# Optimization experiments

Measured on AMD Instinct MI355X. Metric: run time of the kernel, lower is better.

## Reference

```python
import jax, jax.numpy as jnp
import numpy as np
import math

# ---- config (mirrors FastRCNNRoIHeads init args) ----
B, N, C = 8, 2048, 2            # images, proposals/img, classes (incl. background)
K = 100                          # detections_per_img
IMG_H, IMG_W = 512, 512
SCORE_THRESH = 0.05
NMS_THRESH = 0.4
MIN_SIZE = 0.01
WX, WY, WW, WH = 10.0, 10.0, 5.0, 5.0   # BoxCoder weights
BBOX_XFORM_CLIP = math.log(1000.0 / 16.0)


def setup_inputs() -> dict:
    key = jax.random.key(0)
    k1, k2, k3, k4, k5 = jax.random.split(key, 5)
    prop_clss = jax.random.normal(k1, (B, N, C), dtype=jnp.float32)
    prop_regs = 0.1 * jax.random.normal(k2, (B, N, 4), dtype=jnp.float32)
    prop_qlts = jax.random.normal(k3, (B, N, 1), dtype=jnp.float32)
    # valid proposal boxes inside the image: x1,y1 in [0,448), w,h in [16,128)
    xy1 = jax.random.uniform(k4, (B, N, 2), dtype=jnp.float32) * 380.0
    wh = 16.0 + jax.random.uniform(k5, (B, N, 2), dtype=jnp.float32) * 112.0
    props = jnp.concatenate([xy1, xy1 + wh], axis=-1)
    return {"prop_clss": prop_clss, "prop_regs": prop_regs,
            "prop_qlts": prop_qlts, "props": props}


def _decode(regs, props):
    # torchvision BoxCoder.decode_single, class-agnostic [N,4] deltas
    w = props[:, 2] - props[:, 0]
    h = props[:, 3] - props[:, 1]
    cx = props[:, 0] + 0.5 * w
    cy = props[:, 1] + 0.5 * h
    dx, dy = regs[:, 0] / WX, regs[:, 1] / WY
    dw = jnp.minimum(regs[:, 2] / WW, BBOX_XFORM_CLIP)
    dh = jnp.minimum(regs[:, 3] / WH, BBOX_XFORM_CLIP)
    pcx, pcy = dx * w + cx, dy * h + cy
    pw, ph = jnp.exp(dw) * w, jnp.exp(dh) * h
    return jnp.stack([pcx - 0.5 * pw, pcy - 0.5 * ph,
                      pcx + 0.5 * pw, pcy + 0.5 * ph], axis=-1)


def _iou_matrix(b):
    area = (b[:, 2] - b[:, 0]) * (b[:, 3] - b[:, 1])
    lt = jnp.maximum(b[:, None, :2], b[None, :, :2])
    rb = jnp.minimum(b[:, None, 2:], b[None, :, 2:])
    wh = jnp.clip(rb - lt, 0.0)
    inter = wh[..., 0] * wh[..., 1]
    return inter / (area[:, None] + area[None, :] - inter + 1e-9)


def _postprocess_one(clss, regs, qlts, props):
    boxes = _decode(regs, props)
    boxes = jnp.stack([jnp.clip(boxes[:, 0], 0.0, IMG_W),
                       jnp.clip(boxes[:, 1], 0.0, IMG_H),
                       jnp.clip(boxes[:, 2], 0.0, IMG_W),
                       jnp.clip(boxes[:, 3], 0.0, IMG_H)], axis=-1)
    small_ok = ((boxes[:, 2] - boxes[:, 0]) >= MIN_SIZE) & \
               ((boxes[:, 3] - boxes[:, 1]) >= MIN_SIZE)
    raw = jax.nn.softmax(clss, axis=-1)[:, 1:]          # [N, C-1]
    q = jax.nn.sigmoid(qlts[:, 0])                      # [N]
    scores = (q[:, None] * raw).reshape(-1)             # [N*(C-1)]
    raw_f = raw.reshape(-1)
    Cm1 = C - 1
    M = N * Cm1
    prop_idx = jnp.arange(M) // Cm1
    cls_idx = jnp.arange(M) % Cm1 + 1
    valid = (raw_f > SCORE_THRESH) & small_ok[prop_idx]
    cand_boxes = boxes[prop_idx]                        # [M,4]
    # batched_nms: offset boxes per class so NMS runs per class
    max_coord = jnp.max(cand_boxes)
    boxes_off = cand_boxes + (cls_idx.astype(boxes.dtype) * (max_coord + 1.0))[:, None]
    masked = jnp.where(valid, scores, -1.0)
    order = jnp.argsort(-masked)
    b_s = cand_boxes[order]
    bo_s = boxes_off[order]
    s_s = scores[order]
    c_s = cls_idx[order]
    v_s = valid[order]
    iou = _iou_matrix(bo_s)                             # [M,M]
    idxs = jnp.arange(M)

    def step(keep, i):
        sup = (iou[i] > NMS_THRESH) & (idxs > i)
        keep = jnp.where(keep[i], keep & ~sup, keep)
        return keep, None

    keep, _ = jax.lax.scan(step, v_s, idxs)
    rank = jnp.cumsum(keep.astype(jnp.int32)) - 1
    dest = jnp.where(keep & (rank < K), rank, K)        # K = dump slot
    out_b = jnp.zeros((K + 1, 4), boxes.dtype).at[dest].set(b_s)[:K]
    out_s = jnp.zeros((K + 1,), boxes.dtype).at[dest].set(s_s)[:K]
    out_c = jnp.zeros((K + 1,), jnp.int32).at[dest].set(c_s.astype(jnp.int32))[:K]
    return out_b, out_s, out_c


def reference(prop_clss, prop_regs, prop_qlts, props):
    boxes, scores, classes = jax.vmap(_postprocess_one)(
        prop_clss, prop_regs, prop_qlts, props)
    return boxes, scores, classes
```

## Files before the change

### kernel.cpp

```cpp
#include <hip/hip_runtime.h>
#include <stdint.h>

#define NPROP 2048
#define NCLS  2
#define KDET  100
#define BT    512
#define NMS_TH 0.4f

__device__ __forceinline__ float dec_score(uint64_t k) {
    uint32_t u = ~(uint32_t)(k >> 32);
    uint32_t bits = (u & 0x80000000u) ? (u & 0x7FFFFFFFu) : ~u;
    return __uint_as_float(bits);
}

__device__ __forceinline__ float bcastf(float v, int srclane) {
    return __uint_as_float((uint32_t)__builtin_amdgcn_readlane(__float_as_int(v), srclane));
}

__device__ __forceinline__ void decode_one(
    const float* __restrict__ clss, const float* __restrict__ regs,
    const float* __restrict__ qlts, const float* __restrict__ props,
    int b, int i, float4& boxOut, uint64_t& keyOut, float& mxOut)
{
    const float CLIPV = 4.135166556742356f;
    float4 p  = ((const float4*)props)[b * NPROP + i];
    float4 rg = ((const float4*)regs)[b * NPROP + i];
    float2 cc = ((const float2*)clss)[b * NPROP + i];
    float  qv = qlts[(size_t)b * NPROP + i];

    float w  = __fsub_rn(p.z, p.x);
    float h  = __fsub_rn(p.w, p.y);
    float cx = __fadd_rn(p.x, __fmul_rn(0.5f, w));
    float cy = __fadd_rn(p.y, __fmul_rn(0.5f, h));
    float dx = __fdiv_rn(rg.x, 10.0f);
    float dy = __fdiv_rn(rg.y, 10.0f);
    float dw = fminf(__fdiv_rn(rg.z, 5.0f), CLIPV);
    float dh = fminf(__fdiv_rn(rg.w, 5.0f), CLIPV);
    float pcx = __fadd_rn(__fmul_rn(dx, w), cx);
    float pcy = __fadd_rn(__fmul_rn(dy, h), cy);
    float pw  = __fmul_rn(expf(dw), w);
    float ph  = __fmul_rn(expf(dh), h);
    float x1 = __fsub_rn(pcx, __fmul_rn(0.5f, pw));
    float y1 = __fsub_rn(pcy, __fmul_rn(0.5f, ph));
    float x2 = __fadd_rn(pcx, __fmul_rn(0.5f, pw));
    float y2 = __fadd_rn(pcy, __fmul_rn(0.5f, ph));
    x1 = fminf(fmaxf(x1, 0.0f), 512.0f);
    y1 = fminf(fmaxf(y1, 0.0f), 512.0f);
    x2 = fminf(fmaxf(x2, 0.0f), 512.0f);
    y2 = fminf(fmaxf(y2, 0.0f), 512.0f);
    bool small_ok = (__fsub_rn(x2, x1) >= 0.01f) && (__fsub_rn(y2, y1) >= 0.01f);

    float m  = fmaxf(cc.x, cc.y);
    float e0 = expf(__fsub_rn(cc.x, m));
    float e1 = expf(__fsub_rn(cc.y, m));
    float raw = __fdiv_rn(e1, __fadd_rn(e0, e1));
    float sq  = __fdiv_rn(1.0f, __fadd_rn(1.0f, expf(-qv)));
    float score = __fmul_rn(sq, raw);
    bool valid = (raw > 0.05f) && small_ok;
    float masked = valid ? score : -1.0f;

    boxOut = make_float4(x1, y1, x2, y2);
    uint32_t fb = __float_as_uint(masked);
    uint32_t u  = (fb & 0x80000000u) ? ~fb : (fb | 0x80000000u);
    keyOut = ((uint64_t)(~u) << 32) | (uint32_t)i;
    mxOut = fmaxf(fmaxf(x1, y1), fmaxf(x2, y2));
}

__device__ __forceinline__ void bitonic2048(uint64_t key[4], uint64_t* skey,
                                            int idxBase, int lane)
{
    for (int k = 2; k <= NPROP; k <<= 1) {
        for (int j = k >> 1; j > 0; j >>= 1) {
            if (j >= 256) {
                __syncthreads();
#pragma unroll
                for (int r = 0; r < 4; ++r) {
                    int idx = idxBase + r;
                    skey[(idx >> 2) | ((idx & 3) << 9)] = key[r];
                }
                __syncthreads();
#pragma unroll
                for (int r = 0; r < 4; ++r) {
                    int idx  = idxBase + r;
                    int pidx = idx ^ j;
                    uint64_t o = skey[(pidx >> 2) | ((pidx & 3) << 9)];
                    bool takeMin = (((idx & k) == 0) == ((idx & j) == 0));
                    bool lt = key[r] < o;
                    uint64_t mn = lt ? key[r] : o, mx = lt ? o : key[r];
                    key[r] = takeMin ? mn : mx;
                }
            } else if (j >= 4) {
                int lx = j >> 2;
#pragma unroll
                for (int r = 0; r < 4; ++r) {
                    int idx = idxBase + r;
                    uint64_t o = __shfl_xor(key[r], lx, 64);
                    bool takeMin = (((idx & k) == 0) == ((lane & lx) == 0));
                    bool lt = key[r] < o;
                    uint64_t mn = lt ? key[r] : o, mx = lt ? o : key[r];
                    key[r] = takeMin ? mn : mx;
                }
            } else {
#pragma unroll
                for (int r = 0; r < 4; ++r) {
                    if ((r & j) == 0) {
                        int rh = r | j;
                        int idx = idxBase + r;
                        bool up = ((idx & k) == 0);
                        uint64_t a = key[r], c2 = key[rh];
                        bool lt = a < c2;
                        uint64_t mn = lt ? a : c2, mx = lt ? c2 : a;
                        key[r] = up ? mn : mx; key[rh] = up ? mx : mn;
                    }
                }
            }
        }
    }
}

__device__ __forceinline__ int phaseC(
    const uint64_t* keys, int nv, const float4* sboxp, float off,
    uint64_t* s_colpart, uint64_t* s_inpart, float4* s_kbox, float* s_karea,
    int* s_keep, int* s_kept, int lane, int wv)
{
    int c = 0;
    while (true) {
        __syncthreads();
        int kept = *s_kept;
        if (c >= nv || kept >= KDET) break;
        int W = min(64, nv - c);
        bool have = (lane < W);

        float qx1 = 0.f, qy1 = 0.f, qx2 = 0.f, qy2 = 0.f, qa = 0.f;
        if (have) {
            float4 bx = sboxp[(uint32_t)keys[c + lane]];
            qx1 = __fadd_rn(bx.x, off); qy1 = __fadd_rn(bx.y, off);
            qx2 = __fadd_rn(bx.z, off); qy2 = __fadd_rn(bx.w, off);
            qa  = __fmul_rn(__fsub_rn(qx2, qx1), __fsub_rn(qy2, qy1));
        }

        uint64_t colpart = 0;
#pragma unroll
        for (int t = 0; t < 8; ++t) {
            int i = wv + (t << 3);
            bool rowok = (i < W);
            int isrc = rowok ? i : 0;
            float rx1 = bcastf(qx1, isrc);
            float ry1 = bcastf(qy1, isrc);
            float rx2 = bcastf(qx2, isrc);
            float ry2 = bcastf(qy2, isrc);
            float ra  = bcastf(qa , isrc);
            float ltx = fmaxf(rx1, qx1), lty = fmaxf(ry1, qy1);
            float rbx = fminf(rx2, qx2), rby = fminf(ry2, qy2);
            float iw = fmaxf(__fsub_rn(rbx, ltx), 0.0f);
            float ih = fmaxf(__fsub_rn(rby, lty), 0.0f);
            float inter = __fmul_rn(iw, ih);
            float denom = __fadd_rn(__fsub_rn(__fadd_rn(ra, qa), inter), 1e-9f);
            float iou   = __fdiv_rn(inter, denom);
            bool pred = rowok && have && (lane > i) && (iou > NMS_TH);
            uint64_t bm = (uint64_t)__ballot(pred);
            colpart |= ((bm >> lane) & 1ull) << isrc;
        }
        s_colpart[(wv << 6) | lane] = colpart;

        bool supin = false;
        if (have && kept) {
            for (int ki = wv; ki < kept; ki += 8) {
                float4 ko = s_kbox[ki];
                float  ka = s_karea[ki];
                float ltx = fmaxf(ko.x, qx1), lty = fmaxf(ko.y, qy1);
                float rbx = fminf(ko.z, qx2), rby = fminf(ko.w, qy2);
                float iw = fmaxf(__fsub_rn(rbx, ltx), 0.0f);
                float ih = fmaxf(__fsub_rn(rby, lty), 0.0f);
                float inter = __fmul_rn(iw, ih);
                float denom = __fadd_rn(__fsub_rn(__fadd_rn(ka, qa), inter), 1e-9f);
                supin = supin || (__fdiv_rn(inter, denom) > NMS_TH);
            }
        }
        uint64_t inb = (uint64_t)__ballot(supin);
        if (lane == 0) s_inpart[wv] = inb;
        __syncthreads();

        if (wv == 0) {
            uint64_t col = 0, insup = 0;
#pragma unroll
            for (int w2 = 0; w2 < 8; ++w2) {
                col   |= s_colpart[(w2 << 6) | lane];
                insup |= s_inpart[w2];
            }
            bool aliveBit = have && !((insup >> lane) & 1ull);
            uint64_t keepM = (uint64_t)__ballot(aliveBit);
            for (int it = 0; it < 64; ++it) {
                uint64_t nk = (uint64_t)__ballot(aliveBit && ((col & keepM) == 0ull));
                if (nk == keepM) break;
                keepM = nk;
            }
            int quota = KDET - kept;
            int nNew  = __popcll(keepM);
            int take  = nNew < quota ? nNew : quota;
            uint64_t below = keepM & ~(~0ull << lane);
            int rank = __popcll(below);
            bool mine = (((keepM >> lane) & 1ull) != 0ull) && (rank < quota);
            if (mine) {
                s_keep[kept + rank]  = c + lane;
                s_kbox[kept + rank]  = make_float4(qx1, qy1, qx2, qy2);
                s_karea[kept + rank] = qa;
            }
            if (lane == 0) *s_kept = kept + take;
        }
        c += 64;
    }
    __syncthreads();
    return *s_kept;
}

__global__ __launch_bounds__(BT) void PRISM_71511205479155_kernel(
    const float* __restrict__ clss, const float* __restrict__ regs,
    const float* __restrict__ qlts, const float* __restrict__ props,
    float* __restrict__ out, int B)
{
    __shared__ float4   sbox[NPROP];
    __shared__ uint64_t skey[NPROP];
    __shared__ uint64_t cand[512];
    __shared__ uint32_t hist[1024];
    __shared__ uint64_t s_colpart[8 * 64];
    __shared__ uint64_t s_inpart[8];
    __shared__ float4   s_kbox[KDET];
    __shared__ float    s_karea[KDET];
    __shared__ int      s_keep[KDET];
    __shared__ int      s_wsum[8];
    __shared__ int      s_maxc, s_kept, s_beta, s_M, s_totV, s_cnt, s_fb;

    const int b = blockIdx.x, tid = threadIdx.x, lane = tid & 63, wv = tid >> 6;
    const int idxBase = (wv << 8) | (lane << 2);

    hist[tid] = 0; hist[tid + 512] = 0;
    cand[tid] = ~0ull;
    if (tid == 0) { s_maxc = 0; s_kept = 0; s_beta = -1; s_M = 0; s_totV = 0; s_cnt = 0; s_fb = 0; }
    __syncthreads();

    uint64_t key[4];
    float thmax = 0.0f;
#pragma unroll
    for (int r = 0; r < 4; ++r) {
        int i = idxBase + r;
        float4 bx; uint64_t k; float mx;
        decode_one(clss, regs, qlts, props, b, i, bx, k, mx);
        sbox[i] = bx; skey[i] = k; key[r] = k;
        thmax = fmaxf(thmax, mx);
        uint32_t bkt = (uint32_t)(k >> 53);
        if (bkt < 1024)
            atomicAdd(&hist[bkt >> 1], (bkt & 1) ? 0x10000u : 1u);
    }
#pragma unroll
    for (int d = 1; d < 64; d <<= 1) thmax = fmaxf(thmax, __shfl_xor(thmax, d, 64));
    if (lane == 0) atomicMax(&s_maxc, __float_as_int(thmax));
    __syncthreads();

    {
        uint32_t w0 = hist[2 * tid], w1 = hist[2 * tid + 1];
        uint32_t c0 = w0 & 0xFFFFu, c1 = w0 >> 16, c2 = w1 & 0xFFFFu, c3 = w1 >> 16;
        uint32_t local = c0 + c1 + c2 + c3;
        uint32_t incl = local;
#pragma unroll
        for (int d = 1; d < 64; d <<= 1) {
            uint32_t v = __shfl_up(incl, d, 64);
            if (lane >= d) incl += v;
        }
        if (lane == 63) s_wsum[wv] = (int)incl;
        __syncthreads();
        int base = 0, tot = 0;
#pragma unroll
        for (int w = 0; w < 8; ++w) {
            int sv = s_wsum[w];
            tot += sv;
            if (w < wv) base += sv;
        }
        int target = tot < 256 ? tot : 256;
        uint32_t run = (uint32_t)base + incl - local;
        uint32_t cc[4] = {c0, c1, c2, c3};
#pragma unroll
        for (int r = 0; r < 4; ++r) {
            uint32_t ci = run + cc[r];
            if (target > 0 && (int)run < target && (int)ci >= target) {
                s_beta = 4 * tid + r;
                s_M = (int)ci;
                if (ci > 512) s_fb = 1;
            }
            run = ci;
        }
        if (tid == 0) s_totV = tot;
        __syncthreads();
    }

    const float off = __fadd_rn(__int_as_float(s_maxc), 1.0f);
    const int beta = s_beta, M = s_M, totV = s_totV;
    int fb = s_fb;

    if (!fb) {
#pragma unroll
        for (int r = 0; r < 4; ++r) {
            if ((int)(key[r] >> 53) <= beta) {
                int p = atomicAdd(&s_cnt, 1);
                cand[p] = key[r];
            }
        }
        __syncthreads();

        if (wv == 0) {
            uint64_t q[8];
#pragma unroll
            for (int r = 0; r < 8; ++r) q[r] = cand[(lane << 3) | r];
            for (int k2 = 2; k2 <= 512; k2 <<= 1) {
                for (int j = k2 >> 1; j > 0; j >>= 1) {
                    if (j >= 8) {
                        int lx = j >> 3;
#pragma unroll
                        for (int r = 0; r < 8; ++r) {
                            int idx = (lane << 3) | r;
                            uint64_t o = __shfl_xor(q[r], lx, 64);
                            bool takeMin = (((idx & k2) == 0) == ((idx & j) == 0));
                            bool lt = q[r] < o;
                            uint64_t mn = lt ? q[r] : o, mx = lt ? o : q[r];
                            q[r] = takeMin ? mn : mx;
                        }
                    } else {
#pragma unroll
                        for (int r = 0; r < 8; ++r) {
                            if ((r & j) == 0) {
                                int rh = r | j;
                                int idx = (lane << 3) | r;
                                bool up = ((idx & k2) == 0);
                                uint64_t a = q[r], c2 = q[rh];
                                bool lt = a < c2;
                                uint64_t mn = lt ? a : c2, mx = lt ? c2 : a;
                                q[r] = up ? mn : mx; q[rh] = up ? mx : mn;
                            }
                        }
                    }
                }
            }
#pragma unroll
            for (int r = 0; r < 8; ++r) cand[(lane << 3) | r] = q[r];
        }
        __syncthreads();
    }

    int kept = 0;
    if (!fb) kept = phaseC(cand, M, sbox, off, s_colpart, s_inpart,
                           s_kbox, s_karea, s_keep, &s_kept, lane, wv);

    bool needFull = fb || (kept < KDET && M < totV);
    if (needFull) {
        if (tid == 0) s_kept = 0;
        bitonic2048(key, skey, idxBase, lane);
        __syncthreads();
#pragma unroll
        for (int r = 0; r < 4; ++r) skey[idxBase + r] = key[r];
        __syncthreads();
        kept = phaseC(skey, totV, sbox, off, s_colpart, s_inpart,
                      s_kbox, s_karea, s_keep, &s_kept, lane, wv);
    }
    const uint64_t* fkeys = needFull ? skey : cand;

    float* out_boxes  = out;
    float* out_scores = out + (size_t)B * KDET * 4;
    float* out_cls    = out + (size_t)B * KDET * 5;
    for (int s = tid; s < KDET; s += BT) {
        float* ob = out_boxes + ((size_t)b * KDET + s) * 4;
        if (s < kept) {
            uint64_t kk = fkeys[s_keep[s]];
            float4 bx = sbox[(uint32_t)kk];
            ob[0] = bx.x; ob[1] = bx.y; ob[2] = bx.z; ob[3] = bx.w;
            out_scores[(size_t)b * KDET + s] = dec_score(kk);
            out_cls[(size_t)b * KDET + s]    = 1.0f;
        } else {
            ob[0] = 0.0f; ob[1] = 0.0f; ob[2] = 0.0f; ob[3] = 0.0f;
            out_scores[(size_t)b * KDET + s] = 0.0f;
            out_cls[(size_t)b * KDET + s]    = 0.0f;
        }
    }
}

extern "C" void kernel_launch(void* const* d_in, const int* in_sizes, int n_in,
                              void* d_out, int out_size, void* d_ws, size_t ws_size,
                              hipStream_t stream) {
    const float* clss  = (const float*)d_in[0];
    const float* regs  = (const float*)d_in[1];
    const float* qlts  = (const float*)d_in[2];
    const float* props = (const float*)d_in[3];
    float* out = (float*)d_out;

    int B = in_sizes[0] / (NPROP * NCLS);

    PRISM_71511205479155_kernel<<<B, BT, 0, stream>>>(clss, regs, qlts, props, out, B);
}
```

Baseline: 39.75 us.

## Process NMS candidates 128 per round and shrink the candidate sort

The NMS loop now handles two 64-wide chunks per iteration. It computes intra-chunk and cross-chunk IoU bitmasks plus suppression by already-kept boxes for both chunks, which halves the number of barrier-separated rounds. The candidate threshold drops from 256 to 192, so a 256-element wave sort is used when it suffices instead of always sorting 512. Atomic-counter compaction into the candidate buffer is replaced by ballot-based prefix compaction. Shared memory is aliased between histogram, candidate and full-key buffers. The trade-off is more registers and IoU work per round, and more cases may fall back to the full 2048-element sort.

```diff
diff --git a/kernel.cpp b/kernel.cpp
--- a/kernel.cpp
+++ b/kernel.cpp
@@ -15,6 +15,17 @@
 
 __device__ __forceinline__ float bcastf(float v, int srclane) {
     return __uint_as_float((uint32_t)__builtin_amdgcn_readlane(__float_as_int(v), srclane));
+}
+
+__device__ __forceinline__ float iou5(float ax1, float ay1, float ax2, float ay2, float aa,
+                                      float bx1, float by1, float bx2, float by2, float ba) {
+    float ltx = fmaxf(ax1, bx1), lty = fmaxf(ay1, by1);
+    float rbx = fminf(ax2, bx2), rby = fminf(ay2, by2);
+    float iw = fmaxf(__fsub_rn(rbx, ltx), 0.0f);
+    float ih = fmaxf(__fsub_rn(rby, lty), 0.0f);
+    float inter = __fmul_rn(iw, ih);
+    float denom = __fadd_rn(__fsub_rn(__fadd_rn(aa, ba), inter), 1e-9f);
+    return __fdiv_rn(inter, denom);
 }
 
 __device__ __forceinline__ void decode_one(
@@ -118,97 +129,176 @@
     }
 }
 
-__device__ __forceinline__ int phaseC(
+template<int ELEMS, int EPL>
+__device__ __forceinline__ void wavesortN(uint64_t* buf, int lane)
+{
+    uint64_t q[EPL];
+#pragma unroll
+    for (int r = 0; r < EPL; ++r) q[r] = buf[lane * EPL + r];
+    for (int k2 = 2; k2 <= ELEMS; k2 <<= 1) {
+        for (int j = k2 >> 1; j > 0; j >>= 1) {
+            if (j >= EPL) {
+                int lx = j / EPL;
+#pragma unroll
+                for (int r = 0; r < EPL; ++r) {
+                    int idx = lane * EPL + r;
+                    uint64_t o = __shfl_xor(q[r], lx, 64);
+                    bool takeMin = (((idx & k2) == 0) == ((idx & j) == 0));
+                    bool lt = q[r] < o;
+                    uint64_t mn = lt ? q[r] : o, mx = lt ? o : q[r];
+                    q[r] = takeMin ? mn : mx;
+                }
+            } else {
+#pragma unroll
+                for (int r = 0; r < EPL; ++r) {
+                    if ((r & j) == 0) {
+                        int rh = r | j;
+                        int idx = lane * EPL + r;
+                        bool up = ((idx & k2) == 0);
+                        uint64_t a = q[r], c2 = q[rh];
+                        bool lt = a < c2;
+                        uint64_t mn = lt ? a : c2, mx = lt ? c2 : a;
+                        q[r] = up ? mn : mx; q[rh] = up ? mx : mn;
+                    }
+                }
+            }
+        }
+    }
+#pragma unroll
+    for (int r = 0; r < EPL; ++r) buf[lane * EPL + r] = q[r];
+}
+
+__device__ __forceinline__ int phaseC2(
     const uint64_t* keys, int nv, const float4* sboxp, float off,
-    uint64_t* s_colpart, uint64_t* s_inpart, float4* s_kbox, float* s_karea,
-    int* s_keep, int* s_kept, int lane, int wv)
+    uint64_t* s_cp1, uint64_t* s_cpX, uint64_t* s_cp2,
+    uint64_t* s_in1, uint64_t* s_in2,
+    float4* s_kbox, float* s_karea, int* s_keep, int* s_kept, int lane, int wv)
 {
     int c = 0;
     while (true) {
         __syncthreads();
         int kept = *s_kept;
         if (c >= nv || kept >= KDET) break;
-        int W = min(64, nv - c);
-        bool have = (lane < W);
-
-        float qx1 = 0.f, qy1 = 0.f, qx2 = 0.f, qy2 = 0.f, qa = 0.f;
-        if (have) {
+        int W  = nv - c;
+        int W1 = W < 64 ? W : 64;
+        int W2 = (W > 64) ? ((W - 64) < 64 ? (W - 64) : 64) : 0;
+        bool have1 = lane < W1, have2 = lane < W2;
+
+        float ax1=0.f, ay1=0.f, ax2=0.f, ay2=0.f, aa=0.f;
+        float bx1=0.f, by1=0.f, bx2=0.f, by2=0.f, ba=0.f;
+        if (have1) {
             float4 bx = sboxp[(uint32_t)keys[c + lane]];
-            qx1 = __fadd_rn(bx.x, off); qy1 = __fadd_rn(bx.y, off);
-            qx2 = __fadd_rn(bx.z, off); qy2 = __fadd_rn(bx.w, off);
-            qa  = __fmul_rn(__fsub_rn(qx2, qx1), __fsub_rn(qy2, qy1));
-        }
-
-        uint64_t colpart = 0;
+            ax1 = __fadd_rn(bx.x, off); ay1 = __fadd_rn(bx.y, off);
+            ax2 = __fadd_rn(bx.z, off); ay2 = __fadd_rn(bx.w, off);
+            aa  = __fmul_rn(__fsub_rn(ax2, ax1), __fsub_rn(ay2, ay1));
+        }
+        if (have2) {
+            float4 bx = sboxp[(uint32_t)keys[c + 64 + lane]];
+            bx1 = __fadd_rn(bx.x, off); by1 = __fadd_rn(bx.y, off);
+            bx2 = __fadd_rn(bx.z, off); by2 = __fadd_rn(bx.w, off);
+            ba  = __fmul_rn(__fsub_rn(bx2, bx1), __fsub_rn(by2, by1));
+        }
+
+        uint64_t cp1 = 0, cpX = 0, cp2 = 0;
 #pragma unroll
         for (int t = 0; t < 8; ++t) {
             int i = wv + (t << 3);
-            bool rowok = (i < W);
-            int isrc = rowok ? i : 0;
-            float rx1 = bcastf(qx1, isrc);
-            float ry1 = bcastf(qy1, isrc);
-            float rx2 = bcastf(qx2, isrc);
-            float ry2 = bcastf(qy2, isrc);
-            float ra  = bcastf(qa , isrc);
-            float ltx = fmaxf(rx1, qx1), lty = fmaxf(ry1, qy1);
-            float rbx = fminf(rx2, qx2), rby = fminf(ry2, qy2);
-            float iw = fmaxf(__fsub_rn(rbx, ltx), 0.0f);
-            float ih = fmaxf(__fsub_rn(rby, lty), 0.0f);
-            float inter = __fmul_rn(iw, ih);
-            float denom = __fadd_rn(__fsub_rn(__fadd_rn(ra, qa), inter), 1e-9f);
-            float iou   = __fdiv_rn(inter, denom);
-            bool pred = rowok && have && (lane > i) && (iou > NMS_TH);
-            uint64_t bm = (uint64_t)__ballot(pred);
-            colpart |= ((bm >> lane) & 1ull) << isrc;
-        }
-        s_colpart[(wv << 6) | lane] = colpart;
-
-        bool supin = false;
-        if (have && kept) {
+            {
+                bool rowok = (i < W1);
+                int isrc = rowok ? i : 0;
+                float rx1 = bcastf(ax1, isrc), ry1 = bcastf(ay1, isrc);
+                float rx2 = bcastf(ax2, isrc), ry2 = bcastf(ay2, isrc);
+                float ra  = bcastf(aa , isrc);
+                bool p1 = rowok && have1 && (lane > i) &&
+                          (iou5(rx1,ry1,rx2,ry2,ra, ax1,ay1,ax2,ay2,aa) > NMS_TH);
+                uint64_t bm1 = (uint64_t)__ballot(p1);
+                cp1 |= ((bm1 >> lane) & 1ull) << isrc;
+                bool px = rowok && have2 &&
+                          (iou5(rx1,ry1,rx2,ry2,ra, bx1,by1,bx2,by2,ba) > NMS_TH);
+                uint64_t bmx = (uint64_t)__ballot(px);
+                cpX |= ((bmx >> lane) & 1ull) << isrc;
+            }
+            {
+                bool rowok = (i < W2);
+                int isrc = rowok ? i : 0;
+                float rx1 = bcastf(bx1, isrc), ry1 = bcastf(by1, isrc);
+                float rx2 = bcastf(bx2, isrc), ry2 = bcastf(by2, isrc);
+                float ra  = bcastf(ba , isrc);
+                bool p2 = rowok && have2 && (lane > i) &&
+                          (iou5(rx1,ry1,rx2,ry2,ra, bx1,by1,bx2,by2,ba) > NMS_TH);
+                uint64_t bm2 = (uint64_t)__ballot(p2);
+                cp2 |= ((bm2 >> lane) & 1ull) << isrc;
+            }
+        }
+        s_cp1[(wv << 6) | lane] = cp1;
+        s_cpX[(wv << 6) | lane] = cpX;
+        s_cp2[(wv << 6) | lane] = cp2;
+
+        bool si1 = false, si2 = false;
+        if (kept) {
             for (int ki = wv; ki < kept; ki += 8) {
                 float4 ko = s_kbox[ki];
                 float  ka = s_karea[ki];
-                float ltx = fmaxf(ko.x, qx1), lty = fmaxf(ko.y, qy1);
-                float rbx = fminf(ko.z, qx2), rby = fminf(ko.w, qy2);
-                float iw = fmaxf(__fsub_rn(rbx, ltx), 0.0f);
-                float ih = fmaxf(__fsub_rn(rby, lty), 0.0f);
-                float inter = __fmul_rn(iw, ih);
-                float denom = __fadd_rn(__fsub_rn(__fadd_rn(ka, qa), inter), 1e-9f);
-                supin = supin || (__fdiv_rn(inter, denom) > NMS_TH);
-            }
-        }
-        uint64_t inb = (uint64_t)__ballot(supin);
-        if (lane == 0) s_inpart[wv] = inb;
+                si1 = si1 || (have1 && iou5(ko.x,ko.y,ko.z,ko.w,ka, ax1,ay1,ax2,ay2,aa) > NMS_TH);
+                si2 = si2 || (have2 && iou5(ko.x,ko.y,ko.z,ko.w,ka, bx1,by1,bx2,by2,ba) > NMS_TH);
+            }
+        }
+        uint64_t i1b = (uint64_t)__ballot(si1);
+        uint64_t i2b = (uint64_t)__ballot(si2);
+        if (lane == 0) { s_in1[wv] = i1b; s_in2[wv] = i2b; }
         __syncthreads();
 
         if (wv == 0) {
-            uint64_t col = 0, insup = 0;
-#pragma unroll
-            for (int w2 = 0; w2 < 8; ++w2) {
-                col   |= s_colpart[(w2 << 6) | lane];
-                insup |= s_inpart[w2];
-            }
-            bool aliveBit = have && !((insup >> lane) & 1ull);
-            uint64_t keepM = (uint64_t)__ballot(aliveBit);
+            uint64_t col1 = 0, colX = 0, col2 = 0, in1 = 0, in2 = 0;
+#pragma unroll
+            for (int w2i = 0; w2i < 8; ++w2i) {
+                col1 |= s_cp1[(w2i << 6) | lane];
+                colX |= s_cpX[(w2i << 6) | lane];
+                col2 |= s_cp2[(w2i << 6) | lane];
+                in1  |= s_in1[w2i];
+                in2  |= s_in2[w2i];
+            }
+            uint64_t below = ~(~0ull << lane);
+
+            bool alive1 = have1 && !((in1 >> lane) & 1ull);
+            uint64_t keepM1 = (uint64_t)__ballot(alive1);
             for (int it = 0; it < 64; ++it) {
-                uint64_t nk = (uint64_t)__ballot(aliveBit && ((col & keepM) == 0ull));
-                if (nk == keepM) break;
-                keepM = nk;
+                uint64_t nk = (uint64_t)__ballot(alive1 && ((col1 & keepM1) == 0ull));
+                if (nk == keepM1) break;
+                keepM1 = nk;
             }
             int quota = KDET - kept;
-            int nNew  = __popcll(keepM);
-            int take  = nNew < quota ? nNew : quota;
-            uint64_t below = keepM & ~(~0ull << lane);
-            int rank = __popcll(below);
-            bool mine = (((keepM >> lane) & 1ull) != 0ull) && (rank < quota);
-            if (mine) {
-                s_keep[kept + rank]  = c + lane;
-                s_kbox[kept + rank]  = make_float4(qx1, qy1, qx2, qy2);
-                s_karea[kept + rank] = qa;
-            }
-            if (lane == 0) *s_kept = kept + take;
-        }
-        c += 64;
+            int n1 = __popcll(keepM1);
+            int take1 = n1 < quota ? n1 : quota;
+            int rank1 = __popcll(keepM1 & below);
+            if ((((keepM1 >> lane) & 1ull) != 0ull) && rank1 < quota) {
+                s_keep[kept + rank1]  = c + lane;
+                s_kbox[kept + rank1]  = make_float4(ax1, ay1, ax2, ay2);
+                s_karea[kept + rank1] = aa;
+            }
+            int kept1 = kept + take1;
+            int take2 = 0;
+            if (kept1 < KDET && W2 > 0) {
+                bool alive2 = have2 && !((in2 >> lane) & 1ull) && ((colX & keepM1) == 0ull);
+                uint64_t keepM2 = (uint64_t)__ballot(alive2);
+                for (int it = 0; it < 64; ++it) {
+                    uint64_t nk = (uint64_t)__ballot(alive2 && ((col2 & keepM2) == 0ull));
+                    if (nk == keepM2) break;
+                    keepM2 = nk;
+                }
+                int quota2 = KDET - kept1;
+                int n2 = __popcll(keepM2);
+                take2 = n2 < quota2 ? n2 : quota2;
+                int rank2 = __popcll(keepM2 & below);
+                if ((((keepM2 >> lane) & 1ull) != 0ull) && rank2 < quota2) {
+                    s_keep[kept1 + rank2]  = c + 64 + lane;
+                    s_kbox[kept1 + rank2]  = make_float4(bx1, by1, bx2, by2);
+                    s_karea[kept1 + rank2] = ba;
+                }
+            }
+            if (lane == 0) *s_kept = kept1 + take2;
+        }
+        c += 128;
     }
     __syncthreads();
     return *s_kept;
@@ -220,23 +310,26 @@
     float* __restrict__ out, int B)
 {
     __shared__ float4   sbox[NPROP];
-    __shared__ uint64_t skey[NPROP];
-    __shared__ uint64_t cand[512];
-    __shared__ uint32_t hist[1024];
-    __shared__ uint64_t s_colpart[8 * 64];
-    __shared__ uint64_t s_inpart[8];
+    __shared__ __align__(16) char s_reg1[16384];
+    __shared__ uint64_t s_cp1[512];
+    __shared__ uint64_t s_cpX[512];
+    __shared__ uint64_t s_cp2[512];
+    __shared__ uint64_t s_in1[8], s_in2[8];
     __shared__ float4   s_kbox[KDET];
     __shared__ float    s_karea[KDET];
     __shared__ int      s_keep[KDET];
     __shared__ int      s_wsum[8];
-    __shared__ int      s_maxc, s_kept, s_beta, s_M, s_totV, s_cnt, s_fb;
+    __shared__ int      s_maxc, s_kept, s_beta, s_M, s_totV, s_fb;
+
+    uint32_t* hist = (uint32_t*)s_reg1;
+    uint64_t* cand = (uint64_t*)(s_reg1 + 2048);
+    uint64_t* skey = (uint64_t*)s_reg1;
 
     const int b = blockIdx.x, tid = threadIdx.x, lane = tid & 63, wv = tid >> 6;
     const int idxBase = (wv << 8) | (lane << 2);
 
-    hist[tid] = 0; hist[tid + 512] = 0;
-    cand[tid] = ~0ull;
-    if (tid == 0) { s_maxc = 0; s_kept = 0; s_beta = -1; s_M = 0; s_totV = 0; s_cnt = 0; s_fb = 0; }
+    hist[tid & 511] = 0;
+    if (tid == 0) { s_maxc = 0; s_kept = 0; s_beta = -1; s_M = 0; s_totV = 0; s_fb = 0; }
     __syncthreads();
 
     uint64_t key[4];
@@ -246,7 +339,7 @@
         int i = idxBase + r;
         float4 bx; uint64_t k; float mx;
         decode_one(clss, regs, qlts, props, b, i, bx, k, mx);
-        sbox[i] = bx; skey[i] = k; key[r] = k;
+        sbox[i] = bx; key[r] = k;
         thmax = fmaxf(thmax, mx);
         uint32_t bkt = (uint32_t)(k >> 53);
         if (bkt < 1024)
@@ -258,9 +351,9 @@
     __syncthreads();
 
     {
-        uint32_t w0 = hist[2 * tid], w1 = hist[2 * tid + 1];
-        uint32_t c0 = w0 & 0xFFFFu, c1 = w0 >> 16, c2 = w1 & 0xFFFFu, c3 = w1 >> 16;
-        uint32_t local = c0 + c1 + c2 + c3;
+        uint32_t wword = hist[tid & 511];
+        uint32_t c0 = wword & 0xFFFFu, c1 = wword >> 16;
+        uint32_t local = c0 + c1;
         uint32_t incl = local;
 #pragma unroll
         for (int d = 1; d < 64; d <<= 1) {
@@ -276,14 +369,14 @@
             tot += sv;
             if (w < wv) base += sv;
         }
-        int target = tot < 256 ? tot : 256;
+        int target = tot < 192 ? tot : 192;
         uint32_t run = (uint32_t)base + incl - local;
-        uint32_t cc[4] = {c0, c1, c2, c3};
-#pragma unroll
-        for (int r = 0; r < 4; ++r) {
-            uint32_t ci = run + cc[r];
+        uint32_t cc2[2] = {c0, c1};
+#pragma unroll
+        for (int r = 0; r < 2; ++r) {
+            uint32_t ci = run + cc2[r];
             if (target > 0 && (int)run < target && (int)ci >= target) {
-                s_beta = 4 * tid + r;
+                s_beta = 2 * tid + r;
                 s_M = (int)ci;
                 if (ci > 512) s_fb = 1;
             }
@@ -297,58 +390,45 @@
     const int beta = s_beta, M = s_M, totV = s_totV;
     int fb = s_fb;
 
-    if (!fb) {
+    if (!fb && M > 0) {
+        bool pr[4]; uint64_t bal[4]; int wcnt[4];
 #pragma unroll
         for (int r = 0; r < 4; ++r) {
-            if ((int)(key[r] >> 53) <= beta) {
-                int p = atomicAdd(&s_cnt, 1);
-                cand[p] = key[r];
-            }
-        }
+            pr[r]  = ((int)(key[r] >> 53) <= beta);
+            bal[r] = (uint64_t)__ballot(pr[r]);
+            wcnt[r] = __popcll(bal[r]);
+        }
+        int wtot = wcnt[0] + wcnt[1] + wcnt[2] + wcnt[3];
+        if (lane == 0) s_wsum[wv] = wtot;
+        __syncthreads();
+        int base2 = 0;
+#pragma unroll
+        for (int w = 0; w < 8; ++w) if (w < wv) base2 += s_wsum[w];
+        uint64_t below = ~(~0ull << lane);
+        int roff = 0;
+#pragma unroll
+        for (int r = 0; r < 4; ++r) {
+            if (pr[r]) {
+                int pos = base2 + roff + __popcll(bal[r] & below);
+                cand[pos] = key[r];
+            }
+            roff += wcnt[r];
+        }
+        int sortN = (M <= 256) ? 256 : 512;
+        for (int t = M + tid; t < sortN; t += BT) cand[t] = ~0ull;
         __syncthreads();
 
         if (wv == 0) {
-            uint64_t q[8];
-#pragma unroll
-            for (int r = 0; r < 8; ++r) q[r] = cand[(lane << 3) | r];
-            for (int k2 = 2; k2 <= 512; k2 <<= 1) {
-                for (int j = k2 >> 1; j > 0; j >>= 1) {
-                    if (j >= 8) {
-                        int lx = j >> 3;
-#pragma unroll
-                        for (int r = 0; r < 8; ++r) {
-                            int idx = (lane << 3) | r;
-                            uint64_t o = __shfl_xor(q[r], lx, 64);
-                            bool takeMin = (((idx & k2) == 0) == ((idx & j) == 0));
-                            bool lt = q[r] < o;
-                            uint64_t mn = lt ? q[r] : o, mx = lt ? o : q[r];
-                            q[r] = takeMin ? mn : mx;
-                        }
-                    } else {
-#pragma unroll
-                        for (int r = 0; r < 8; ++r) {
-                            if ((r & j) == 0) {
-                                int rh = r | j;
-                                int idx = (lane << 3) | r;
-                                bool up = ((idx & k2) == 0);
-                                uint64_t a = q[r], c2 = q[rh];
-                                bool lt = a < c2;
-                                uint64_t mn = lt ? a : c2, mx = lt ? c2 : a;
-                                q[r] = up ? mn : mx; q[rh] = up ? mx : mn;
-                            }
-                        }
-                    }
-                }
-            }
-#pragma unroll
-            for (int r = 0; r < 8; ++r) cand[(lane << 3) | r] = q[r];
+            if (sortN == 256) wavesortN<256, 4>(cand, lane);
+            else              wavesortN<512, 8>(cand, lane);
         }
         __syncthreads();
     }
 
     int kept = 0;
-    if (!fb) kept = phaseC(cand, M, sbox, off, s_colpart, s_inpart,
-                           s_kbox, s_karea, s_keep, &s_kept, lane, wv);
+    if (!fb && M > 0)
+        kept = phaseC2(cand, M, sbox, off, s_cp1, s_cpX, s_cp2, s_in1, s_in2,
+                       s_kbox, s_karea, s_keep, &s_kept, lane, wv);
 
     bool needFull = fb || (kept < KDET && M < totV);
     if (needFull) {
@@ -357,9 +437,8 @@
         __syncthreads();
 #pragma unroll
         for (int r = 0; r < 4; ++r) skey[idxBase + r] = key[r];
-        __syncthreads();
-        kept = phaseC(skey, totV, sbox, off, s_colpart, s_inpart,
-                      s_kbox, s_karea, s_keep, &s_kept, lane, wv);
+        kept = phaseC2(skey, totV, sbox, off, s_cp1, s_cpX, s_cp2, s_in1, s_in2,
+                       s_kbox, s_karea, s_keep, &s_kept, lane, wv);
     }
     const uint64_t* fkeys = needFull ? skey : cand;
 
```

Result: faster. 33.86 us (-14.8%).
